# Optimization experiments

Measured on AMD Instinct MI355X. Metric: run time of the kernel, lower is better.

## Reference

```python
import jax, jax.numpy as jnp
import numpy as np

N, E, F, H, G = 50000, 1600000, 128, 128, 64
EPS = 1e-5  # BatchNorm eps


def setup_inputs() -> dict:
    key = jax.random.key(0)
    ks = jax.random.split(key, 16)
    x = jax.random.normal(ks[0], (N, F), dtype=jnp.float32)
    edge_index = jax.random.randint(ks[1], (2, E), 0, N, dtype=jnp.int64)
    batch = jnp.sort(jax.random.randint(ks[2], (N,), 0, G, dtype=jnp.int64))
    inp = {
        'x': x, 'edge_index': edge_index, 'batch': batch,
        'W1': jax.random.normal(ks[3], (F, H), dtype=jnp.float32) / np.sqrt(F),
        'b1': jnp.zeros((H,), jnp.float32),
        'bn1_gamma': jax.random.uniform(ks[4], (H,), jnp.float32, 0.5, 1.5),
        'bn1_beta': jax.random.normal(ks[5], (H,), jnp.float32) * 0.1,
        'bn1_mean': jax.random.normal(ks[6], (H,), jnp.float32) * 0.1,
        'bn1_var': jax.random.uniform(ks[7], (H,), jnp.float32, 0.5, 1.5),
        'W2': jax.random.normal(ks[8], (H, H), dtype=jnp.float32) / np.sqrt(H),
        'b2': jnp.zeros((H,), jnp.float32),
        'bn2_gamma': jax.random.uniform(ks[9], (H,), jnp.float32, 0.5, 1.5),
        'bn2_beta': jax.random.normal(ks[10], (H,), jnp.float32) * 0.1,
        'bn2_mean': jax.random.normal(ks[11], (H,), jnp.float32) * 0.1,
        'bn2_var': jax.random.uniform(ks[12], (H,), jnp.float32, 0.5, 1.5),
        'att_w': jax.random.normal(ks[13], (H, 1), dtype=jnp.float32) / np.sqrt(H),
        'cls_w': jax.random.normal(ks[14], (1, H), dtype=jnp.float32) / np.sqrt(H),
        'cls_b': jnp.zeros((1,), jnp.float32),
    }
    return inp


def gcn_conv(h, W, b, src, dst, n):
    # PyG GCNConv: linear, add self-loops, symmetric D^{-1/2}(A+I)D^{-1/2} aggregation, bias.
    hw = h @ W                                   # [n, H]
    loops = jnp.arange(n, dtype=src.dtype)
    s = jnp.concatenate([src, loops])
    d = jnp.concatenate([dst, loops])
    deg = jax.ops.segment_sum(jnp.ones_like(d, dtype=hw.dtype), d, num_segments=n)
    dis = jnp.where(deg > 0, jax.lax.rsqrt(deg), 0.0)
    norm = dis[s] * dis[d]                       # [E+n]
    msgs = hw[s] * norm[:, None]                 # gather + scale (memory-bound)
    return jax.ops.segment_sum(msgs, d, num_segments=n) + b


def batch_norm(h, gamma, beta, mean, var):
    return (h - mean) * gamma * jax.lax.rsqrt(var + EPS) + beta


def reference(x, edge_index, batch, W1, b1, bn1_gamma, bn1_beta, bn1_mean, bn1_var,
              W2, b2, bn2_gamma, bn2_beta, bn2_mean, bn2_var, att_w, cls_w, cls_b):
    n = x.shape[0]
    src, dst = edge_index[0], edge_index[1]
    # eval mode: dropout and edge-dropout are no-ops; BN uses running stats
    h = gcn_conv(x, W1, b1, src, dst, n)
    h = jax.nn.relu(batch_norm(h, bn1_gamma, bn1_beta, bn1_mean, bn1_var))
    h = gcn_conv(h, W2, b2, src, dst, n)
    h = jax.nn.relu(batch_norm(h, bn2_gamma, bn2_beta, bn2_mean, bn2_var))
    att = jax.nn.sigmoid(h @ att_w)              # [n, 1]
    g = jax.ops.segment_sum(h * att, batch, num_segments=G)  # [G, H]
    logits = g @ cls_w.T + cls_b                 # [G, 1]
    return logits, att
```

## Files before the change

### kernel.cpp

```cpp
#include <hip/hip_runtime.h>
#include <math.h>

#define NN 50000
#define HID 128
#define NG 64
#define BN_EPS 1e-5f

typedef __attribute__((ext_vector_type(8))) short short8;
typedef __attribute__((ext_vector_type(4))) float f32x4;

__device__ inline unsigned pack_bf2(float a, float b) {
    union { float f; unsigned u; } ua, ub;
    ua.f = a; ub.f = b;
    unsigned x = ua.u, y = ub.u;
    x += 0x7fffu + ((x >> 16) & 1u);
    y += 0x7fffu + ((y >> 16) & 1u);
    return (x >> 16) | (y & 0xffff0000u);
}
__device__ inline unsigned short bf16_1(float x) {
    union { float f; unsigned u; } v;
    v.f = x;
    unsigned r = v.u + 0x7fffu + ((v.u >> 16) & 1u);
    return (unsigned short)(r >> 16);
}
__device__ inline float2 unpack_bf2(unsigned v) {
    union { unsigned u; float f; } a, b;
    a.u = v << 16;
    b.u = v & 0xffff0000u;
    return make_float2(a.f, b.f);
}

#define NBKT 256
#define ETILE 4096
#define EPT   (ETILE / 256)
#define CAP   8192
#define ASTR 136

__global__ __launch_bounds__(128) void k_prep0(const float* __restrict__ W1,
                                               const float* __restrict__ W2,
                                               unsigned short* __restrict__ wt1,
                                               unsigned short* __restrict__ wt2,
                                               int* __restrict__ bcurP,
                                               const float* __restrict__ cls_b,
                                               float* __restrict__ logits) {
    int b = blockIdx.x;
    int t = threadIdx.x;
    if (b < 256) {
        int k = b & 127;
        const float* W = (b < 128) ? W1 : W2;
        unsigned short* wt = (b < 128) ? wt1 : wt2;
        wt[t * 128 + k] = bf16_1(W[k * 128 + t]);
    } else {
        #pragma unroll
        for (int i = 0; i < 32; ++i) bcurP[t * 32 + i] = 0;
        if (t < NG) logits[t] = cls_b[0];
    }
}

struct SmemDist {
    int h[NBKT], sx[NBKT], cur[NBKT], gb[NBKT];
    unsigned stage[ETILE];
};

__global__ __launch_bounds__(256) void k_dist_gemm1(const int* __restrict__ src,
                                                    const int* __restrict__ dst,
                                                    int* __restrict__ bcurP,
                                                    unsigned* __restrict__ bpacked,
                                                    const float* __restrict__ x,
                                                    const unsigned short* __restrict__ wt1,
                                                    unsigned short* __restrict__ zb,
                                                    int E, int K, int n, int DB) {
    __shared__ __align__(16) char smem[sizeof(SmemDist)];
    int t = threadIdx.x;
    int b = blockIdx.x;

    if (b < DB) {
        SmemDist* s = (SmemDist*)smem;
        s->h[t] = 0;
        __syncthreads();
        int base = b * ETILE;
        int dreg[EPT];
        #pragma unroll
        for (int i = 0; i < EPT; ++i) {
            int e = base + i * 256 + t;
            dreg[i] = (e < E) ? dst[e] : -1;
            if (dreg[i] >= 0) atomicAdd(&s->h[dreg[i] / K], 1);
        }
        __syncthreads();
        int c = s->h[t];
        s->sx[t] = c;
        __syncthreads();
        for (int off = 1; off < NBKT; off <<= 1) {
            int v = (t >= off) ? s->sx[t - off] : 0;
            __syncthreads();
            s->sx[t] += v;
            __syncthreads();
        }
        int nvalid = s->sx[NBKT - 1];
        int excl = s->sx[t] - c;
        __syncthreads();
        s->sx[t] = excl;
        s->cur[t] = excl;
        s->gb[t] = (c > 0) ? atomicAdd(&bcurP[t * 16], c) : 0;
        __syncthreads();
        #pragma unroll
        for (int i = 0; i < EPT; ++i) {
            int e = base + i * 256 + t;
            if (dreg[i] >= 0) {
                int d = dreg[i];
                int bkt = d / K;
                int p = atomicAdd(&s->cur[bkt], 1);
                s->stage[p] = ((unsigned)d << 16) | (unsigned)src[e];
            }
        }
        __syncthreads();
        for (int idx = t; idx < nvalid; idx += 256) {
            unsigned v = s->stage[idx];
            int bkt = (int)(v >> 16) / K;
            int pos = s->gb[bkt] + (idx - s->sx[bkt]);
            bpacked[(size_t)bkt * CAP + pos] = v;
        }
        return;
    }

    typedef unsigned short ArowT[ASTR];
    ArowT* A = (ArowT*)smem;
    int row0 = (b - DB) * 64;
    #pragma unroll
    for (int i = 0; i < 8; ++i) {
        int idx = t + i * 256;
        int r = idx >> 5;
        int c4 = (idx & 31) * 4;
        float4 v = make_float4(0.f, 0.f, 0.f, 0.f);
        if (row0 + r < n) v = *(const float4*)&x[(size_t)(row0 + r) * 128 + c4];
        uint2 p;
        p.x = pack_bf2(v.x, v.y);
        p.y = pack_bf2(v.z, v.w);
        *(uint2*)&A[r][c4] = p;
    }
    __syncthreads();
    int lane = t & 63;
    int wave = t >> 6;
    int m = lane & 15;
    int quad = lane >> 4;
    int r0 = wave * 16;
    short8 a[4];
    #pragma unroll
    for (int kt = 0; kt < 4; ++kt)
        a[kt] = *(const short8*)&A[r0 + m][kt * 32 + quad * 8];
    f32x4 acc[8];
    #pragma unroll
    for (int ct = 0; ct < 8; ++ct) acc[ct] = (f32x4){0.f, 0.f, 0.f, 0.f};
    short8 bcur[4], bnxt[4];
    {
        const unsigned short* wb = &wt1[(size_t)m * 128 + quad * 8];
        #pragma unroll
        for (int kt = 0; kt < 4; ++kt) bcur[kt] = *(const short8*)(wb + kt * 32);
    }
    #pragma unroll
    for (int ct = 0; ct < 8; ++ct) {
        if (ct < 7) {
            const unsigned short* wb = &wt1[(size_t)((ct + 1) * 16 + m) * 128 + quad * 8];
            #pragma unroll
            for (int kt = 0; kt < 4; ++kt) bnxt[kt] = *(const short8*)(wb + kt * 32);
        }
        #pragma unroll
        for (int kt = 0; kt < 4; ++kt)
            acc[ct] = __builtin_amdgcn_mfma_f32_16x16x32_bf16(a[kt], bcur[kt], acc[ct], 0, 0, 0);
        #pragma unroll
        for (int kt = 0; kt < 4; ++kt) bcur[kt] = bnxt[kt];
    }
    __syncthreads();
    #pragma unroll
    for (int ct = 0; ct < 8; ++ct) {
        int col = ct * 16 + m;
        #pragma unroll
        for (int reg = 0; reg < 4; ++reg)
            A[r0 + quad * 4 + reg][col] = bf16_1(acc[ct][reg]);
    }
    __syncthreads();
    #pragma unroll
    for (int i = 0; i < 4; ++i) {
        int idx = t + i * 256;
        int r = idx >> 4;
        int c8 = (idx & 15) * 8;
        int grow = row0 + r;
        if (grow < n)
            *(uint4*)&zb[(size_t)grow * 128 + c8] = *(const uint4*)&A[r][c8];
    }
}

__global__ __launch_bounds__(256) void k_csr_scale(const unsigned* __restrict__ bpacked,
                                                   const int* __restrict__ bcurP,
                                                   int* __restrict__ row_ptr,
                                                   int* __restrict__ degA,
                                                   float* __restrict__ dis,
                                                   unsigned short* __restrict__ col16,
                                                   unsigned short* __restrict__ zb,
                                                   int n, int K) {
    __shared__ int cnt[NBKT];
    __shared__ int sA[NBKT];
    __shared__ int cur[NBKT];
    __shared__ float disL[NBKT];
    __shared__ unsigned short stage[CAP];
    int t = threadIdx.x;
    int b = blockIdx.x;
    int node0 = b * K;
    int nn = n - node0;
    if (nn > K) nn = K;
    if (nn < 0) nn = 0;
    int e0 = b * CAP;
    int ne = bcurP[b * 16];
    cnt[t] = 0;
    __syncthreads();
    int n4 = (ne + 3) >> 2;
    for (int i = t; i < n4; i += 256) {
        uint4 v = *(const uint4*)&bpacked[e0 + 4 * i];
        int rem = ne - 4 * i;
        if (rem > 0) atomicAdd(&cnt[(int)(v.x >> 16) - node0], 1);
        if (rem > 1) atomicAdd(&cnt[(int)(v.y >> 16) - node0], 1);
        if (rem > 2) atomicAdd(&cnt[(int)(v.z >> 16) - node0], 1);
        if (rem > 3) atomicAdd(&cnt[(int)(v.w >> 16) - node0], 1);
    }
    __syncthreads();
    int c = cnt[t];
    sA[t] = c;
    __syncthreads();
    for (int off = 1; off < NBKT; off <<= 1) {
        int v = (t >= off) ? sA[t - off] : 0;
        __syncthreads();
        sA[t] += v;
        __syncthreads();
    }
    int excl = sA[t] - c;
    cur[t] = excl;
    float dv = rsqrtf((float)(c + 1));
    disL[t] = dv;
    if (t < nn) {
        row_ptr[node0 + t] = e0 + excl;
        degA[node0 + t] = c;
        dis[node0 + t] = dv;
    }
    __syncthreads();
    for (int i = t; i < n4; i += 256) {
        uint4 v = *(const uint4*)&bpacked[e0 + 4 * i];
        int rem = ne - 4 * i;
        unsigned vv[4] = {v.x, v.y, v.z, v.w};
        #pragma unroll
        for (int j = 0; j < 4; ++j) {
            if (rem > j) {
                int ld = (int)(vv[j] >> 16) - node0;
                int p = atomicAdd(&cur[ld], 1);
                stage[p] = (unsigned short)(vv[j] & 0xFFFFu);
            }
        }
    }
    __syncthreads();
    int nw = (ne + 1) >> 1;
    for (int i = t; i < nw; i += 256) {
        unsigned w = (unsigned)stage[2 * i] | ((unsigned)stage[2 * i + 1] << 16);
        *(unsigned*)&col16[e0 + 2 * i] = w;
    }
    for (int idx = t; idx < nn * 16; idx += 256) {
        int r = idx >> 4;
        int c8 = (idx & 15) * 8;
        float sc = disL[r];
        size_t o8 = (size_t)(node0 + r) * 128 + c8;
        uint4 v = *(const uint4*)&zb[o8];
        unsigned* w = (unsigned*)&v;
        #pragma unroll
        for (int k2 = 0; k2 < 4; ++k2) {
            float2 f = unpack_bf2(w[k2]);
            w[k2] = pack_bf2(f.x * sc, f.y * sc);
        }
        *(uint4*)&zb[o8] = v;
    }
}


__device__ __forceinline__ void gather_pipe(const unsigned short* __restrict__ hws,
                                            const unsigned short* __restrict__ col16,
                                            int e0, int deg, int md, int sl, int part,
                                            float* acc8) {
    int nt = (md + 7) >> 3;
    if (nt <= 0) return;
    int base = part << 4;
    uint4 vA[8], vB[8];
    int c0, c1, n0 = 0, n1 = 0;
    c0 = (sl < deg) ? (int)col16[e0 + sl] : 0;
    c1 = (sl + 16 < deg) ? (int)col16[e0 + 16 + sl] : 0;

    #pragma unroll
    for (int j = 0; j < 8; ++j) {
        int s = __shfl(c0, base + j);
        vA[j] = (j < deg) ? *(const uint4*)(hws + ((size_t)s << 7) + (sl << 3))
                          : make_uint4(0, 0, 0, 0);
    }
    int t = 0, ebase = 0;
    for (;;) {
        if (t + 4 < nt) {
            n0 = (ebase + 32 + sl < deg) ? (int)col16[e0 + ebase + 32 + sl] : 0;
            n1 = (ebase + 48 + sl < deg) ? (int)col16[e0 + ebase + 48 + sl] : 0;
        }
        if (t + 1 < nt) {
            int it0 = (t + 1) << 3;
            #pragma unroll
            for (int j = 0; j < 8; ++j) {
                int s = __shfl(c0, base + 8 + j);
                vB[j] = (it0 + j < deg) ? *(const uint4*)(hws + ((size_t)s << 7) + (sl << 3))
                                        : make_uint4(0, 0, 0, 0);
            }
        }
        #pragma unroll
        for (int j = 0; j < 8; ++j) {
            const unsigned* w = (const unsigned*)&vA[j];
            #pragma unroll
            for (int i2 = 0; i2 < 4; ++i2) {
                float2 f = unpack_bf2(w[i2]);
                acc8[2 * i2]     += f.x;
                acc8[2 * i2 + 1] += f.y;
            }
        }
        if (++t >= nt) break;
        if (t + 1 < nt) {
            int it0 = (t + 1) << 3;
            #pragma unroll
            for (int j = 0; j < 8; ++j) {
                int s = __shfl(c1, base + j);
                vA[j] = (it0 + j < deg) ? *(const uint4*)(hws + ((size_t)s << 7) + (sl << 3))
                                        : make_uint4(0, 0, 0, 0);
            }
        }
        #pragma unroll
        for (int j = 0; j < 8; ++j) {
            const unsigned* w = (const unsigned*)&vB[j];
            #pragma unroll
            for (int i2 = 0; i2 < 4; ++i2) {
                float2 f = unpack_bf2(w[i2]);
                acc8[2 * i2]     += f.x;
                acc8[2 * i2 + 1] += f.y;
            }
        }
        if (++t >= nt) break;
        if (t + 1 < nt) {
            int it0 = (t + 1) << 3;
            #pragma unroll
            for (int j = 0; j < 8; ++j) {
                int s = __shfl(c1, base + 8 + j);
                vB[j] = (it0 + j < deg) ? *(const uint4*)(hws + ((size_t)s << 7) + (sl << 3))
                                        : make_uint4(0, 0, 0, 0);
            }
        }
        #pragma unroll
        for (int j = 0; j < 8; ++j) {
            const unsigned* w = (const unsigned*)&vA[j];
            #pragma unroll
            for (int i2 = 0; i2 < 4; ++i2) {
                float2 f = unpack_bf2(w[i2]);
                acc8[2 * i2]     += f.x;
                acc8[2 * i2 + 1] += f.y;
            }
        }
        if (++t >= nt) break;
        if (t + 1 < nt) {
            int it0 = (t + 1) << 3;
            #pragma unroll
            for (int j = 0; j < 8; ++j) {
                int s = __shfl(n0, base + j);
                vA[j] = (it0 + j < deg) ? *(const uint4*)(hws + ((size_t)s << 7) + (sl << 3))
                                        : make_uint4(0, 0, 0, 0);
            }
        }
        #pragma unroll
        for (int j = 0; j < 8; ++j) {
            const unsigned* w = (const unsigned*)&vB[j];
            #pragma unroll
            for (int i2 = 0; i2 < 4; ++i2) {
                float2 f = unpack_bf2(w[i2]);
                acc8[2 * i2]     += f.x;
                acc8[2 * i2 + 1] += f.y;
            }
        }
        if (++t >= nt) break;
        c0 = n0; c1 = n1; ebase += 32;
    }
}


__global__ __launch_bounds__(256, 3) void k_agg1_gemm2(const unsigned short* __restrict__ zb,
                                                       const int* __restrict__ row_ptr,
                                                       const int* __restrict__ degA,
                                                       const unsigned short* __restrict__ col16,
                                                       const float* __restrict__ dis,
                                                       const float* __restrict__ bias,
                                                       const float* __restrict__ gamma,
                                                       const float* __restrict__ beta,
                                                       const float* __restrict__ mean,
                                                       const float* __restrict__ var,
                                                       const unsigned short* __restrict__ wt2,
                                                       unsigned short* __restrict__ hwsb2, int n) {
    __shared__ unsigned short H1[16][ASTR];
    __shared__ unsigned short C2[16][ASTR];
    int t = threadIdx.x;
    int wave = t >> 6, lane = t & 63;
    int sl = lane & 15, part = lane >> 4;
    int d = blockIdx.x * 16 + wave * 4 + part;
    bool active = (d < n);
    int e0 = 0, deg = 0;
    if (active) {
        e0 = row_ptr[d];
        deg = degA[d];
    }
    uint4 vs = make_uint4(0, 0, 0, 0);
    float dd = 0.f;
    if (active) {
        vs = *(const uint4*)(zb + ((size_t)d << 7) + (sl << 3));
        dd = dis[d];
    }
    int md = deg;
    md = max(md, __shfl_xor(md, 16));
    md = max(md, __shfl_xor(md, 32));

    float acc8[8] = {0, 0, 0, 0, 0, 0, 0, 0};
    gather_pipe(zb, col16, e0, deg, md, sl, part, acc8);

    unsigned outw[4] = {0, 0, 0, 0};
    if (active) {
        const unsigned* w = (const unsigned*)&vs;
        #pragma unroll
        for (int i2 = 0; i2 < 4; ++i2) {
            float2 f = unpack_bf2(w[i2]);
            acc8[2 * i2]     += f.x;
            acc8[2 * i2 + 1] += f.y;
        }
        int f0 = sl << 3;
        #pragma unroll
        for (int i2 = 0; i2 < 4; ++i2) {
            int f = f0 + 2 * i2;
            float2 bv = *(const float2*)&bias[f];
            float2 gm = *(const float2*)&gamma[f];
            float2 bt = *(const float2*)&beta[f];
            float2 mn = *(const float2*)&mean[f];
            float2 vr = *(const float2*)&var[f];
            float vx = acc8[2 * i2] * dd + bv.x;
            float vy = acc8[2 * i2 + 1] * dd + bv.y;
            float sx = gm.x * rsqrtf(vr.x + BN_EPS);
            float sy = gm.y * rsqrtf(vr.y + BN_EPS);
            float rx = fmaxf((vx - mn.x) * sx + bt.x, 0.f);
            float ry = fmaxf((vy - mn.y) * sy + bt.y, 0.f);
            outw[i2] = pack_bf2(rx, ry);
        }
    }
    int local = wave * 4 + part;
    *(uint4*)&H1[local][sl << 3] = *(uint4*)outw;
    __syncthreads();

    int m = sl;
    int quad = part;
    short8 a2[4];
    #pragma unroll
    for (int kt = 0; kt < 4; ++kt)
        a2[kt] = *(const short8*)&H1[m][kt * 32 + quad * 8];

    f32x4 acc2[2];
    acc2[0] = (f32x4){0.f, 0.f, 0.f, 0.f};
    acc2[1] = (f32x4){0.f, 0.f, 0.f, 0.f};
    #pragma unroll
    for (int i = 0; i < 2; ++i) {
        int ct = wave * 2 + i;
        const unsigned short* wb = &wt2[(size_t)(ct * 16 + m) * 128 + quad * 8];
        #pragma unroll
        for (int kt = 0; kt < 4; ++kt) {
            short8 b = *(const short8*)(wb + kt * 32);
            acc2[i] = __builtin_amdgcn_mfma_f32_16x16x32_bf16(a2[kt], b, acc2[i], 0, 0, 0);
        }
    }
    int gr = blockIdx.x * 16 + quad * 4;
    float ds2[4];
    #pragma unroll
    for (int reg = 0; reg < 4; ++reg)
        ds2[reg] = (gr + reg < n) ? dis[gr + reg] : 0.f;
    #pragma unroll
    for (int i = 0; i < 2; ++i) {
        int col = (wave * 2 + i) * 16 + m;
        #pragma unroll
        for (int reg = 0; reg < 4; ++reg)
            C2[quad * 4 + reg][col] = bf16_1(acc2[i][reg] * ds2[reg]);
    }
    __syncthreads();
    {
        int r = t >> 4;
        int c8 = (t & 15) * 8;
        int grow = blockIdx.x * 16 + r;
        if (grow < n)
            *(uint4*)&hwsb2[(size_t)grow * 128 + c8] = *(const uint4*)&C2[r][c8];
    }
}


__global__ __launch_bounds__(256, 3) void k_agg2_att_logit(const unsigned short* __restrict__ hwsb,
                                                           const int* __restrict__ row_ptr,
                                                           const int* __restrict__ degA,
                                                           const unsigned short* __restrict__ col16,
                                                           const float* __restrict__ dis,
                                                           const float* __restrict__ bias,
                                                           const float* __restrict__ gamma,
                                                           const float* __restrict__ beta,
                                                           const float* __restrict__ mean,
                                                           const float* __restrict__ var,
                                                           const int* __restrict__ batch,
                                                           const float* __restrict__ att_w,
                                                           const float* __restrict__ cls_w,
                                                           float* __restrict__ att_out,
                                                           float* __restrict__ logits, int n) {
    __shared__ int   sg[16];
    __shared__ float sv[16];
    int t = threadIdx.x;
    int wave = t >> 6, lane = t & 63;
    int sl = lane & 15, part = lane >> 4;
    int d = blockIdx.x * 16 + wave * 4 + part;
    bool active = (d < n);
    int e0 = 0, deg = 0;
    if (active) {
        e0 = row_ptr[d];
        deg = degA[d];
    }
    uint4 vs = make_uint4(0, 0, 0, 0);
    float dd = 0.f;
    int g = -1;
    if (active) {
        vs = *(const uint4*)(hwsb + ((size_t)d << 7) + (sl << 3));
        dd = dis[d];
        g = batch[d];
    }
    int md = deg;
    md = max(md, __shfl_xor(md, 16));
    md = max(md, __shfl_xor(md, 32));

    float acc8[8] = {0, 0, 0, 0, 0, 0, 0, 0};
    gather_pipe(hwsb, col16, e0, deg, md, sl, part, acc8);

    float contrib = 0.f;
    float p = 0.f, q = 0.f;
    if (active) {
        const unsigned* w = (const unsigned*)&vs;
        #pragma unroll
        for (int i2 = 0; i2 < 4; ++i2) {
            float2 f = unpack_bf2(w[i2]);
            acc8[2 * i2]     += f.x;
            acc8[2 * i2 + 1] += f.y;
        }
        int f0 = sl << 3;
        #pragma unroll
        for (int i2 = 0; i2 < 4; ++i2) {
            int f = f0 + 2 * i2;
            float2 bv = *(const float2*)&bias[f];
            float2 gm = *(const float2*)&gamma[f];
            float2 bt = *(const float2*)&beta[f];
            float2 mn = *(const float2*)&mean[f];
            float2 vr = *(const float2*)&var[f];
            float vx = acc8[2 * i2] * dd + bv.x;
            float vy = acc8[2 * i2 + 1] * dd + bv.y;
            float sx = gm.x * rsqrtf(vr.x + BN_EPS);
            float sy = gm.y * rsqrtf(vr.y + BN_EPS);
            float rx = fmaxf((vx - mn.x) * sx + bt.x, 0.f);
            float ry = fmaxf((vy - mn.y) * sy + bt.y, 0.f);
            float2 aw = *(const float2*)&att_w[f];
            float2 cw = *(const float2*)&cls_w[f];
            p += rx * aw.x + ry * aw.y;
            q += rx * cw.x + ry * cw.y;
        }
    }
    #pragma unroll
    for (int off = 1; off < 16; off <<= 1) {
        p += __shfl_xor(p, off);
        q += __shfl_xor(q, off);
    }
    if (active) {
        float a = 1.f / (1.f + expf(-p));
        if (sl == 0) att_out[d] = a;
        contrib = a * q;
    }
    if (sl == 0) {
        sg[wave * 4 + part] = g;
        sv[wave * 4 + part] = contrib;
    }
    __syncthreads();
    if (t == 0) {
        int cur = -1;
        float acc = 0.f;
        #pragma unroll
        for (int i = 0; i < 16; ++i) {
            int gi = sg[i];
            if (gi < 0) continue;
            if (gi != cur) {
                if (cur >= 0) atomicAdd(&logits[cur], acc);
                cur = gi;
                acc = 0.f;
            }
            acc += sv[i];
        }
        if (cur >= 0) atomicAdd(&logits[cur], acc);
    }
}


extern "C" void kernel_launch(void* const* d_in, const int* in_sizes, int n_in,
                              void* d_out, int out_size, void* d_ws, size_t ws_size,
                              hipStream_t stream) {
    const float* x   = (const float*)d_in[0];
    const int*   ei  = (const int*)d_in[1];
    const int*   bat = (const int*)d_in[2];
    const float* W1  = (const float*)d_in[3];
    const float* b1  = (const float*)d_in[4];
    const float* g1  = (const float*)d_in[5];
    const float* bt1 = (const float*)d_in[6];
    const float* mn1 = (const float*)d_in[7];
    const float* vr1 = (const float*)d_in[8];
    const float* W2  = (const float*)d_in[9];
    const float* b2  = (const float*)d_in[10];
    const float* g2  = (const float*)d_in[11];
    const float* bt2 = (const float*)d_in[12];
    const float* mn2 = (const float*)d_in[13];
    const float* vr2 = (const float*)d_in[14];
    const float* attw = (const float*)d_in[15];
    const float* clsw = (const float*)d_in[16];
    const float* clsb = (const float*)d_in[17];

    int E = in_sizes[1] / 2;
    int n = in_sizes[2];
    const int* src = ei;
    const int* dst = ei + E;
    int K = (n + NBKT - 1) / NBKT;

    char* ws = (char*)d_ws;
    auto alloc = [&](size_t bytes) {
        void* p = (void*)ws;
        ws += (bytes + 255) & ~(size_t)255;
        return p;
    };
    int*            bcurP   = (int*)alloc(NBKT * 16 * 4);
    unsigned*       bpacked = (unsigned*)alloc((size_t)NBKT * CAP * 4);
    int*            row_ptr = (int*)alloc((size_t)n * 4);
    int*            degA    = (int*)alloc((size_t)n * 4);
    unsigned short* col16   = (unsigned short*)alloc(((size_t)NBKT * CAP + 1024) * 2);
    float*          dis     = (float*)alloc((size_t)n * 4);
    unsigned short* zb      = (unsigned short*)alloc((size_t)n * 128 * 2);
    unsigned short* hwsb2   = (unsigned short*)alloc((size_t)n * 128 * 2);
    unsigned short* wt1     = (unsigned short*)alloc(128 * 128 * 2);
    unsigned short* wt2     = (unsigned short*)alloc(128 * 128 * 2);

    float* out = (float*)d_out;
    int DB = (E + ETILE - 1) / ETILE;
    int gb = (n + 63) / 64;
    int ab = (n + 15) / 16;

    k_prep0<<<257, 128, 0, stream>>>(W1, W2, wt1, wt2, bcurP, clsb, out);
    k_dist_gemm1<<<DB + gb, 256, 0, stream>>>(src, dst, bcurP, bpacked, x, wt1, zb,
                                              E, K, n, DB);
    k_csr_scale<<<NBKT, 256, 0, stream>>>(bpacked, bcurP, row_ptr, degA, dis,
                                          col16, zb, n, K);
    k_agg1_gemm2<<<ab, 256, 0, stream>>>(zb, row_ptr, degA, col16, dis,
                                         b1, g1, bt1, mn1, vr1, wt2, hwsb2, n);
    k_agg2_att_logit<<<ab, 256, 0, stream>>>(hwsb2, row_ptr, degA, col16, dis,
                                             b2, g2, bt2, mn2, vr2, bat, attw, clsw,
                                             out + NG, out, n);
}
```

Before: 267.7 us.

## Split GEMM1 across dist and CSR kernels, move row scaling to separate kernel

The first GEMM's row tiles are split in half: one half runs alongside edge bucketing, the other alongside CSR construction, so both sort-like kernels get dense work to overlap with their atomics and scans. Bucketing switches to fixed 256-node buckets with shifts and masks instead of a runtime divisor. CAP grows to 10240 to absorb the larger per-bucket edge counts. Degree scaling of zb moves to its own elementwise kernel, which adds a launch and an extra pass over zb.

```diff
diff --git a/kernel.cpp b/kernel.cpp
--- a/kernel.cpp
+++ b/kernel.cpp
@@ -33,7 +33,7 @@
 #define NBKT 256
 #define ETILE 4096
 #define EPT   (ETILE / 256)
-#define CAP   8192
+#define CAP   10240
 #define ASTR 136
 
 __global__ __launch_bounds__(128) void k_prep0(const float* __restrict__ W1,
@@ -57,75 +57,13 @@
     }
 }
 
-struct SmemDist {
-    int h[NBKT], sx[NBKT], cur[NBKT], gb[NBKT];
-    unsigned stage[ETILE];
-};
-
-__global__ __launch_bounds__(256) void k_dist_gemm1(const int* __restrict__ src,
-                                                    const int* __restrict__ dst,
-                                                    int* __restrict__ bcurP,
-                                                    unsigned* __restrict__ bpacked,
-                                                    const float* __restrict__ x,
-                                                    const unsigned short* __restrict__ wt1,
-                                                    unsigned short* __restrict__ zb,
-                                                    int E, int K, int n, int DB) {
-    __shared__ __align__(16) char smem[sizeof(SmemDist)];
-    int t = threadIdx.x;
-    int b = blockIdx.x;
-
-    if (b < DB) {
-        SmemDist* s = (SmemDist*)smem;
-        s->h[t] = 0;
-        __syncthreads();
-        int base = b * ETILE;
-        int dreg[EPT];
-        #pragma unroll
-        for (int i = 0; i < EPT; ++i) {
-            int e = base + i * 256 + t;
-            dreg[i] = (e < E) ? dst[e] : -1;
-            if (dreg[i] >= 0) atomicAdd(&s->h[dreg[i] / K], 1);
-        }
-        __syncthreads();
-        int c = s->h[t];
-        s->sx[t] = c;
-        __syncthreads();
-        for (int off = 1; off < NBKT; off <<= 1) {
-            int v = (t >= off) ? s->sx[t - off] : 0;
-            __syncthreads();
-            s->sx[t] += v;
-            __syncthreads();
-        }
-        int nvalid = s->sx[NBKT - 1];
-        int excl = s->sx[t] - c;
-        __syncthreads();
-        s->sx[t] = excl;
-        s->cur[t] = excl;
-        s->gb[t] = (c > 0) ? atomicAdd(&bcurP[t * 16], c) : 0;
-        __syncthreads();
-        #pragma unroll
-        for (int i = 0; i < EPT; ++i) {
-            int e = base + i * 256 + t;
-            if (dreg[i] >= 0) {
-                int d = dreg[i];
-                int bkt = d / K;
-                int p = atomicAdd(&s->cur[bkt], 1);
-                s->stage[p] = ((unsigned)d << 16) | (unsigned)src[e];
-            }
-        }
-        __syncthreads();
-        for (int idx = t; idx < nvalid; idx += 256) {
-            unsigned v = s->stage[idx];
-            int bkt = (int)(v >> 16) / K;
-            int pos = s->gb[bkt] + (idx - s->sx[bkt]);
-            bpacked[(size_t)bkt * CAP + pos] = v;
-        }
-        return;
-    }
-
+__device__ __forceinline__ void gemm1_tile(char* smem, int row0,
+                                           const float* __restrict__ x,
+                                           const unsigned short* __restrict__ wt1,
+                                           unsigned short* __restrict__ zb,
+                                           int n, int t) {
     typedef unsigned short ArowT[ASTR];
     ArowT* A = (ArowT*)smem;
-    int row0 = (b - DB) * 64;
     #pragma unroll
     for (int i = 0; i < 8; ++i) {
         int idx = t + i * 256;
@@ -190,56 +128,131 @@
     }
 }
 
-__global__ __launch_bounds__(256) void k_csr_scale(const unsigned* __restrict__ bpacked,
+struct SmemDist {
+    int h[NBKT], sx[NBKT], cur[NBKT], gb[NBKT];
+    unsigned stage[ETILE];
+};
+
+__global__ __launch_bounds__(256) void k_dist_gemm1(const int* __restrict__ src,
+                                                    const int* __restrict__ dst,
+                                                    int* __restrict__ bcurP,
+                                                    unsigned* __restrict__ bpacked,
+                                                    const float* __restrict__ x,
+                                                    const unsigned short* __restrict__ wt1,
+                                                    unsigned short* __restrict__ zb,
+                                                    int E, int n, int DB) {
+    __shared__ __align__(16) char smem[sizeof(SmemDist)];
+    int t = threadIdx.x;
+    int b = blockIdx.x;
+
+    if (b >= DB) {
+        gemm1_tile(smem, (b - DB) * 64, x, wt1, zb, n, t);
+        return;
+    }
+    SmemDist* s = (SmemDist*)smem;
+    s->h[t] = 0;
+    __syncthreads();
+    int base = b * ETILE;
+    int dreg[EPT];
+    #pragma unroll
+    for (int i = 0; i < EPT; ++i) {
+        int e = base + i * 256 + t;
+        dreg[i] = (e < E) ? dst[e] : -1;
+        if (dreg[i] >= 0) atomicAdd(&s->h[dreg[i] >> 8], 1);
+    }
+    __syncthreads();
+    int c = s->h[t];
+    s->sx[t] = c;
+    __syncthreads();
+    for (int off = 1; off < NBKT; off <<= 1) {
+        int v = (t >= off) ? s->sx[t - off] : 0;
+        __syncthreads();
+        s->sx[t] += v;
+        __syncthreads();
+    }
+    int nvalid = s->sx[NBKT - 1];
+    int excl = s->sx[t] - c;
+    __syncthreads();
+    s->sx[t] = excl;
+    s->cur[t] = excl;
+    s->gb[t] = (c > 0) ? atomicAdd(&bcurP[t * 16], c) : 0;
+    __syncthreads();
+    #pragma unroll
+    for (int i = 0; i < EPT; ++i) {
+        int e = base + i * 256 + t;
+        if (dreg[i] >= 0) {
+            int d = dreg[i];
+            int bkt = d >> 8;
+            int p = atomicAdd(&s->cur[bkt], 1);
+            s->stage[p] = ((unsigned)d << 16) | (unsigned)src[e];
+        }
+    }
+    __syncthreads();
+    for (int idx = t; idx < nvalid; idx += 256) {
+        unsigned v = s->stage[idx];
+        int bkt = (int)(v >> 24);
+        int pos = s->gb[bkt] + (idx - s->sx[bkt]);
+        bpacked[(size_t)bkt * CAP + pos] = v;
+    }
+}
+
+struct SmemCSR {
+    int cnt[NBKT], sA[NBKT], cur[NBKT];
+    unsigned short stage[CAP];
+};
+
+__global__ __launch_bounds__(256) void k_csr_gemm1(const unsigned* __restrict__ bpacked,
                                                    const int* __restrict__ bcurP,
                                                    int* __restrict__ row_ptr,
                                                    int* __restrict__ degA,
                                                    float* __restrict__ dis,
                                                    unsigned short* __restrict__ col16,
+                                                   const float* __restrict__ x,
+                                                   const unsigned short* __restrict__ wt1,
                                                    unsigned short* __restrict__ zb,
-                                                   int n, int K) {
-    __shared__ int cnt[NBKT];
-    __shared__ int sA[NBKT];
-    __shared__ int cur[NBKT];
-    __shared__ float disL[NBKT];
-    __shared__ unsigned short stage[CAP];
+                                                   int n, int NB, int row0B) {
+    __shared__ __align__(16) char smem[sizeof(SmemCSR)];
     int t = threadIdx.x;
     int b = blockIdx.x;
-    int node0 = b * K;
+
+    if (b >= NB) {
+        gemm1_tile(smem, row0B + (b - NB) * 64, x, wt1, zb, n, t);
+        return;
+    }
+    SmemCSR* s = (SmemCSR*)smem;
+    int node0 = b << 8;
     int nn = n - node0;
-    if (nn > K) nn = K;
+    if (nn > 256) nn = 256;
     if (nn < 0) nn = 0;
     int e0 = b * CAP;
     int ne = bcurP[b * 16];
-    cnt[t] = 0;
+    s->cnt[t] = 0;
     __syncthreads();
     int n4 = (ne + 3) >> 2;
     for (int i = t; i < n4; i += 256) {
         uint4 v = *(const uint4*)&bpacked[e0 + 4 * i];
         int rem = ne - 4 * i;
-        if (rem > 0) atomicAdd(&cnt[(int)(v.x >> 16) - node0], 1);
-        if (rem > 1) atomicAdd(&cnt[(int)(v.y >> 16) - node0], 1);
-        if (rem > 2) atomicAdd(&cnt[(int)(v.z >> 16) - node0], 1);
-        if (rem > 3) atomicAdd(&cnt[(int)(v.w >> 16) - node0], 1);
-    }
-    __syncthreads();
-    int c = cnt[t];
-    sA[t] = c;
+        if (rem > 0) atomicAdd(&s->cnt[(v.x >> 16) & 255u], 1);
+        if (rem > 1) atomicAdd(&s->cnt[(v.y >> 16) & 255u], 1);
+        if (rem > 2) atomicAdd(&s->cnt[(v.z >> 16) & 255u], 1);
+        if (rem > 3) atomicAdd(&s->cnt[(v.w >> 16) & 255u], 1);
+    }
+    __syncthreads();
+    int c = s->cnt[t];
+    s->sA[t] = c;
     __syncthreads();
     for (int off = 1; off < NBKT; off <<= 1) {
-        int v = (t >= off) ? sA[t - off] : 0;
+        int v = (t >= off) ? s->sA[t - off] : 0;
         __syncthreads();
-        sA[t] += v;
+        s->sA[t] += v;
         __syncthreads();
     }
-    int excl = sA[t] - c;
-    cur[t] = excl;
-    float dv = rsqrtf((float)(c + 1));
-    disL[t] = dv;
+    int excl = s->sA[t] - c;
+    s->cur[t] = excl;
     if (t < nn) {
         row_ptr[node0 + t] = e0 + excl;
         degA[node0 + t] = c;
-        dis[node0 + t] = dv;
+        dis[node0 + t] = rsqrtf((float)(c + 1));
     }
     __syncthreads();
     for (int i = t; i < n4; i += 256) {
@@ -249,32 +262,35 @@
         #pragma unroll
         for (int j = 0; j < 4; ++j) {
             if (rem > j) {
-                int ld = (int)(vv[j] >> 16) - node0;
-                int p = atomicAdd(&cur[ld], 1);
-                stage[p] = (unsigned short)(vv[j] & 0xFFFFu);
+                int ld = (int)((vv[j] >> 16) & 255u);
+                int p = atomicAdd(&s->cur[ld], 1);
+                s->stage[p] = (unsigned short)(vv[j] & 0xFFFFu);
             }
         }
     }
     __syncthreads();
     int nw = (ne + 1) >> 1;
     for (int i = t; i < nw; i += 256) {
-        unsigned w = (unsigned)stage[2 * i] | ((unsigned)stage[2 * i + 1] << 16);
+        unsigned w = (unsigned)s->stage[2 * i] | ((unsigned)s->stage[2 * i + 1] << 16);
         *(unsigned*)&col16[e0 + 2 * i] = w;
     }
-    for (int idx = t; idx < nn * 16; idx += 256) {
-        int r = idx >> 4;
-        int c8 = (idx & 15) * 8;
-        float sc = disL[r];
-        size_t o8 = (size_t)(node0 + r) * 128 + c8;
-        uint4 v = *(const uint4*)&zb[o8];
-        unsigned* w = (unsigned*)&v;
-        #pragma unroll
-        for (int k2 = 0; k2 < 4; ++k2) {
-            float2 f = unpack_bf2(w[k2]);
-            w[k2] = pack_bf2(f.x * sc, f.y * sc);
-        }
-        *(uint4*)&zb[o8] = v;
-    }
+}
+
+__global__ __launch_bounds__(256) void k_scale(unsigned short* __restrict__ zb,
+                                               const float* __restrict__ dis, int n) {
+    int i = blockIdx.x * 256 + threadIdx.x;
+    int r = i >> 4;
+    if (r >= n) return;
+    int c8 = (i & 15) * 8;
+    float s = dis[r];
+    uint4 v = *(const uint4*)&zb[(size_t)r * 128 + c8];
+    unsigned* w = (unsigned*)&v;
+    #pragma unroll
+    for (int k = 0; k < 4; ++k) {
+        float2 f = unpack_bf2(w[k]);
+        w[k] = pack_bf2(f.x * s, f.y * s);
+    }
+    *(uint4*)&zb[(size_t)r * 128 + c8] = v;
 }
 
 
@@ -631,7 +647,7 @@
     int n = in_sizes[2];
     const int* src = ei;
     const int* dst = ei + E;
-    int K = (n + NBKT - 1) / NBKT;
+    int NB = (n + 255) >> 8;
 
     char* ws = (char*)d_ws;
     auto alloc = [&](size_t bytes) {
@@ -653,13 +669,17 @@
     float* out = (float*)d_out;
     int DB = (E + ETILE - 1) / ETILE;
     int gb = (n + 63) / 64;
+    int G1A = gb / 2;
+    int G1B = gb - G1A;
     int ab = (n + 15) / 16;
+    int sb = (n * 16 + 255) / 256;
 
     k_prep0<<<257, 128, 0, stream>>>(W1, W2, wt1, wt2, bcurP, clsb, out);
-    k_dist_gemm1<<<DB + gb, 256, 0, stream>>>(src, dst, bcurP, bpacked, x, wt1, zb,
-                                              E, K, n, DB);
-    k_csr_scale<<<NBKT, 256, 0, stream>>>(bpacked, bcurP, row_ptr, degA, dis,
-                                          col16, zb, n, K);
+    k_dist_gemm1<<<DB + G1A, 256, 0, stream>>>(src, dst, bcurP, bpacked, x, wt1, zb,
+                                               E, n, DB);
+    k_csr_gemm1<<<NB + G1B, 256, 0, stream>>>(bpacked, bcurP, row_ptr, degA, dis,
+                                              col16, x, wt1, zb, n, NB, G1A * 64);
+    k_scale<<<sb, 256, 0, stream>>>(zb, dis, n);
     k_agg1_gemm2<<<ab, 256, 0, stream>>>(zb, row_ptr, degA, col16, dis,
                                          b1, g1, bt1, mn1, vr1, wt2, hwsb2, n);
     k_agg2_att_logit<<<ab, 256, 0, stream>>>(hwsb2, row_ptr, degA, col16, dis,
```

After: 265.1 us. No clear change (-1.0%).
